# Performance work log

Hardware: AMD Instinct MI355X
Metric: run time of the kernel (lower is better)

Reference implementation:

```python
import jax, jax.numpy as jnp
import numpy as np

MARGIN = 0.2  # contrastive margin
# sim_type_dot = 'MISA': max over image regions, mean over (valid) words


def setup_inputs() -> dict:
    key = jax.random.key(0)
    k1, k2, k3, k4 = jax.random.split(key, 4)
    B, R, W, D = 128, 36, 60, 1024
    im = jax.random.normal(k1, (B, R, D), dtype=jnp.float32)
    s = jax.random.normal(k2, (B, W, D), dtype=jnp.float32)
    x = jax.random.normal(k3, (B, W, D), dtype=jnp.float32)  # unused in math, kept for API fidelity
    s_l = jax.random.randint(k4, (B,), 1, W + 1)  # caption lengths in [1, W]
    return {"im": im, "s": s, "s_l": s_l, "x": x}


def _scores(im, s, s_l):
    # im: (B, R, D) images; s: (B, W, D) captions; s_l: (B,) lengths
    B, W = s.shape[0], s.shape[1]
    # matchmap M[i, j, r, w] = <image j region r, caption i word w>
    M = jnp.einsum('jrd,iwd->ijrw', im, s)
    # MISA: max over regions r, then mean over the n_word valid words of caption i
    M_max = M.max(axis=2)                                   # (i, j, w)
    word_mask = (jnp.arange(W)[None, :] < s_l[:, None]).astype(M.dtype)  # (i, w)
    sims = (M_max * word_mask[:, None, :]).sum(axis=-1) / s_l[:, None].astype(M.dtype)  # (i, j)
    # original layout: scores[image j, caption i]
    return sims.T


def reference(im, s, s_l, x):
    scores = _scores(im, s, s_l)                 # (B, B)
    diag = jnp.diagonal(scores)[:, None]         # (B, 1)
    cost_s = jnp.maximum(MARGIN + scores - diag, 0.0)
    cost_im = jnp.maximum(MARGIN + scores - diag.T, 0.0)
    eye = jnp.eye(scores.shape[0], dtype=bool)
    cost_s = jnp.where(eye, 0.0, cost_s)
    cost_im = jnp.where(eye, 0.0, cost_im)
    return cost_s.sum() + cost_im.sum()
```

## Files before the change

### kernel.cpp

```cpp
#include <hip/hip_runtime.h>
#include <hip/hip_bf16.h>
#include <stdint.h>

#define B_SZ 128
#define R_SZ 36
#define RP_SZ 48
#define W_SZ 60
#define WP_SZ 64
#define D_SZ 1024
#define MARGIN 0.2f

#define ATILE_B (192 * 64)
#define BTILE_B (256 * 64)

typedef __attribute__((ext_vector_type(4))) float f32x4;
typedef __attribute__((ext_vector_type(2))) long longx2;

typedef __attribute__((address_space(3))) unsigned int lds_u32;
typedef const __attribute__((address_space(1))) unsigned int glb_u32;

__device__ __forceinline__ void gload16(const unsigned char* g, unsigned char* l) {
    __builtin_amdgcn_global_load_lds((glb_u32*)g, (lds_u32*)l, 16, 0, 0);
}

__global__ __launch_bounds__(256) void convert_fp8_kernel(
        const float* __restrict__ im, const float* __restrict__ s,
        unsigned char* __restrict__ imb, unsigned char* __restrict__ sb) {
    const int nA = B_SZ * RP_SZ * 64;
    const int nB = B_SZ * WP_SZ * 64;
    int i = blockIdx.x * 256 + threadIdx.x;
    const float* srcrow;
    unsigned char* dst;
    int gran, row;
    if (i < nA) {
        gran = i & 63; row = i >> 6;
        int j = row / RP_SZ, r = row % RP_SZ;
        int rs = r < R_SZ ? r : R_SZ - 1;
        srcrow = im + ((size_t)(j * R_SZ + rs) << 10);
        dst = imb + (size_t)i * 16;
    } else {
        int i2 = i - nA;
        if (i2 >= nB) return;
        gran = i2 & 63; row = i2 >> 6;
        int j = row >> 6, w = row & 63;
        int ws = w < W_SZ ? w : W_SZ - 1;
        srcrow = s + ((size_t)(j * W_SZ + ws) << 10);
        dst = sb + (size_t)i2 * 16;
    }
    const int kb = gran >> 2, g = gran & 3;
    uint4 o;
    unsigned int* op = (unsigned int*)&o;
#pragma unroll
    for (int q = 0; q < 4; ++q) {
        const int kq = kb * 64 + (q >> 1) * 32 + g * 8 + (q & 1) * 4;
        float4 v = *reinterpret_cast<const float4*>(srcrow + kq);
        int w32 = __builtin_amdgcn_cvt_pk_fp8_f32(v.x, v.y, 0, false);
        w32 = __builtin_amdgcn_cvt_pk_fp8_f32(v.z, v.w, w32, true);
        op[q] = (unsigned int)w32;
    }
    *reinterpret_cast<uint4*>(dst) = o;
}

__global__ __launch_bounds__(512, 2) void scores_kernel(
        const unsigned char* __restrict__ imb,
        const unsigned char* __restrict__ sb,
        const int* __restrict__ s_l,
        float* __restrict__ S)
{
    __shared__ __align__(16) unsigned char As[2 * ATILE_B];
    __shared__ __align__(16) unsigned char Bs[2 * BTILE_B];

    const int tid  = threadIdx.x;
    const int wid  = tid >> 6;
    const int lane = tid & 63;
    const int l15  = lane & 15;
    const int kgrp = lane >> 4;
    const int wr   = wid >> 2;
    const int wc   = wid & 3;

    int bid = blockIdx.x;
    int k8  = bid & 7;
    int w   = bid >> 3;
    int jtg = w >> 5;
    int sw  = w & 31;
    int it  = k8 * 4 + (sw >> 3);
    int jt  = jtg * 8 + (sw & 7);

    const int drow = lane >> 2;
    const int sgr  = ((lane & 3) ^ ((lane >> 3) & 3)) * 16;

    const unsigned char* gsrc[4];
    unsigned char* gdst0[4];
    int tsz[4];
#pragma unroll
    for (int si = 0; si < 4; ++si) {
        int c = wid + si * 8;
        if (c < 12) {
            gsrc[si]  = imb + (size_t)(jt * 192 + c * 16 + drow) * 1024 + sgr;
            gdst0[si] = As + c * 1024 + lane * 16;
            tsz[si]   = ATILE_B;
        } else if (c < 28) {
            int b = c - 12;
            gsrc[si]  = sb + (size_t)(it * 256 + b * 16 + drow) * 1024 + sgr;
            gdst0[si] = Bs + b * 1024 + lane * 16;
            tsz[si]   = BTILE_B;
        }
    }

    const int slot0 = (kgrp ^ ((l15 >> 1) & 3)) * 16;
    int abase[6];
#pragma unroll
    for (int rf = 0; rf < 6; ++rf)
        abase[rf] = (wr * 96 + rf * 16 + l15) * 64 + slot0;
    int bbase[4];
#pragma unroll
    for (int cf = 0; cf < 4; ++cf)
        bbase[cf] = (wc * 64 + cf * 16 + l15) * 64 + slot0;

    f32x4 acc[6][4] = {};

#pragma unroll
    for (int si = 0; si < 4; ++si) {
        int c = wid + si * 8;
        if (c < 28) gload16(gsrc[si], gdst0[si]);
    }
    asm volatile("s_waitcnt vmcnt(0)" ::: "memory");
    __builtin_amdgcn_s_barrier();

#pragma unroll 2
    for (int kt = 0; kt < 16; ++kt) {
        const int cur = kt & 1;
        const unsigned char* Ac = As + cur * ATILE_B;
        const unsigned char* Bc = Bs + cur * BTILE_B;

        longx2 afr[6], bfr[4];
#pragma unroll
        for (int rf = 0; rf < 6; ++rf)
            afr[rf] = *reinterpret_cast<const longx2*>(Ac + abase[rf]);
#pragma unroll
        for (int cf = 0; cf < 4; ++cf)
            bfr[cf] = *reinterpret_cast<const longx2*>(Bc + bbase[cf]);

        if (kt < 15) {
            const int ko = (kt + 1) * 64;
            const int nb = cur ^ 1;
#pragma unroll
            for (int si = 0; si < 4; ++si) {
                int c = wid + si * 8;
                if (c < 28) gload16(gsrc[si] + ko, gdst0[si] + nb * tsz[si]);
            }
        }

        __builtin_amdgcn_s_setprio(1);
#pragma unroll
        for (int k2 = 0; k2 < 2; ++k2)
#pragma unroll
            for (int rf = 0; rf < 6; ++rf)
#pragma unroll
                for (int cf = 0; cf < 4; ++cf)
                    acc[rf][cf] = __builtin_amdgcn_mfma_f32_16x16x32_fp8_fp8(
                        afr[rf][k2], bfr[cf][k2], acc[rf][cf], 0, 0, 0);
        __builtin_amdgcn_s_setprio(0);

        if (kt < 15) {
            asm volatile("s_waitcnt vmcnt(0)" ::: "memory");
            __builtin_amdgcn_s_barrier();
        }
    }

    const int i_cap = it * 4 + wc;
    const int nw = s_l[i_cap];
    const float inv = 1.0f / (float)nw;
#pragma unroll
    for (int h = 0; h < 2; ++h) {
        float sum = 0.0f;
#pragma unroll
        for (int cf = 0; cf < 4; ++cf) {
            float m = acc[h * 3][cf][0];
#pragma unroll
            for (int rf = h * 3; rf < h * 3 + 3; ++rf)
#pragma unroll
                for (int e = 0; e < 4; ++e)
                    m = fmaxf(m, acc[rf][cf][e]);
            m = fmaxf(m, __shfl_xor(m, 16));
            m = fmaxf(m, __shfl_xor(m, 32));
            int wv = cf * 16 + l15;
            if (wv < nw) sum += m;
        }
        sum += __shfl_xor(sum, 1);
        sum += __shfl_xor(sum, 2);
        sum += __shfl_xor(sum, 4);
        sum += __shfl_xor(sum, 8);
        if (lane == 0) {
            int j_img = jt * 4 + wr * 2 + h;
            S[j_img * B_SZ + i_cap] = sum * inv;
        }
    }
}

__global__ __launch_bounds__(1024) void loss_kernel(
        const float* __restrict__ S, float* __restrict__ out) {
    __shared__ float diag[B_SZ];
    __shared__ float red[1024];
    int t = threadIdx.x;
    if (t < B_SZ) diag[t] = S[t * (B_SZ + 1)];
    __syncthreads();
    float acc = 0.0f;
    for (int idx = t; idx < B_SZ * B_SZ; idx += 1024) {
        int a = idx >> 7, b = idx & (B_SZ - 1);
        if (a != b) {
            float v = S[idx];
            acc += fmaxf(MARGIN + v - diag[a], 0.0f)
                 + fmaxf(MARGIN + v - diag[b], 0.0f);
        }
    }
    red[t] = acc;
    __syncthreads();
    for (int s = 512; s > 0; s >>= 1) {
        if (t < s) red[t] += red[t + s];
        __syncthreads();
    }
    if (t == 0) out[0] = red[0];
}

extern "C" void kernel_launch(void* const* d_in, const int* in_sizes, int n_in,
                              void* d_out, int out_size, void* d_ws, size_t ws_size,
                              hipStream_t stream) {
    const float* im  = (const float*)d_in[0];
    const float* s   = (const float*)d_in[1];
    const int*   s_l = (const int*)d_in[2];

    const int n_im_pad = B_SZ * RP_SZ * D_SZ;
    const int n_s_pad  = B_SZ * WP_SZ * D_SZ;

    unsigned char* imb = (unsigned char*)d_ws;
    unsigned char* sb  = imb + n_im_pad;
    float* S = (float*)(sb + n_s_pad);

    const int ngran = (n_im_pad + n_s_pad) / 16;
    convert_fp8_kernel<<<(ngran + 255) / 256, 256, 0, stream>>>(im, s, imb, sb);

    scores_kernel<<<1024, 512, 0, stream>>>(imb, sb, s_l, S);

    loss_kernel<<<1, 1024, 0, stream>>>(S, (float*)d_out);
}
```

Baseline: 86.44 us.

## Prefetch two K-tiles ahead and register double-buffer LDS fragments in GEMM loop

Restructures the main K loop of the fp8 scores GEMM. Global-to-LDS loads now run two tiles ahead, and LDS fragments for the next tile are read into a second register set while the second half of the current tile's MFMAs executes. The goal is to hide global-load and LDS latency behind matrix work instead of stalling at the start of each tile. The cost is more live registers (two fragment sets), and the final steps issue a redundant reload of tile 15. It also relies on careful vmcnt and barrier ordering to avoid races on the buffer being overwritten.

```diff
diff --git a/kernel.cpp b/kernel.cpp
--- a/kernel.cpp
+++ b/kernel.cpp
@@ -118,55 +118,73 @@
         bbase[cf] = (wc * 64 + cf * 16 + l15) * 64 + slot0;
 
     f32x4 acc[6][4] = {};
+    longx2 fa[6], fb[4], ga[6], gb[4];
 
 #pragma unroll
     for (int si = 0; si < 4; ++si) {
         int c = wid + si * 8;
         if (c < 28) gload16(gsrc[si], gdst0[si]);
     }
-    asm volatile("s_waitcnt vmcnt(0)" ::: "memory");
+#pragma unroll
+    for (int si = 0; si < 4; ++si) {
+        int c = wid + si * 8;
+        if (c < 28) gload16(gsrc[si] + 64, gdst0[si] + tsz[si]);
+    }
+    asm volatile("s_waitcnt vmcnt(7)" ::: "memory");
     __builtin_amdgcn_s_barrier();
-
-#pragma unroll 2
-    for (int kt = 0; kt < 16; ++kt) {
-        const int cur = kt & 1;
-        const unsigned char* Ac = As + cur * ATILE_B;
-        const unsigned char* Bc = Bs + cur * BTILE_B;
-
-        longx2 afr[6], bfr[4];
-#pragma unroll
-        for (int rf = 0; rf < 6; ++rf)
-            afr[rf] = *reinterpret_cast<const longx2*>(Ac + abase[rf]);
-#pragma unroll
-        for (int cf = 0; cf < 4; ++cf)
-            bfr[cf] = *reinterpret_cast<const longx2*>(Bc + bbase[cf]);
-
-        if (kt < 15) {
-            const int ko = (kt + 1) * 64;
-            const int nb = cur ^ 1;
-#pragma unroll
-            for (int si = 0; si < 4; ++si) {
-                int c = wid + si * 8;
-                if (c < 28) gload16(gsrc[si] + ko, gdst0[si] + nb * tsz[si]);
-            }
-        }
-
-        __builtin_amdgcn_s_setprio(1);
-#pragma unroll
-        for (int k2 = 0; k2 < 2; ++k2)
-#pragma unroll
-            for (int rf = 0; rf < 6; ++rf)
-#pragma unroll
-                for (int cf = 0; cf < 4; ++cf)
-                    acc[rf][cf] = __builtin_amdgcn_mfma_f32_16x16x32_fp8_fp8(
-                        afr[rf][k2], bfr[cf][k2], acc[rf][cf], 0, 0, 0);
-        __builtin_amdgcn_s_setprio(0);
-
-        if (kt < 15) {
-            asm volatile("s_waitcnt vmcnt(0)" ::: "memory");
-            __builtin_amdgcn_s_barrier();
-        }
-    }
+#pragma unroll
+    for (int rf = 0; rf < 6; ++rf)
+        fa[rf] = *reinterpret_cast<const longx2*>(As + abase[rf]);
+#pragma unroll
+    for (int cf = 0; cf < 4; ++cf)
+        fb[cf] = *reinterpret_cast<const longx2*>(Bs + bbase[cf]);
+
+#define TILE_STEP(t, CA, CB, NA, NB)                                           \
+    {                                                                          \
+        const int cur = (t) & 1;                                               \
+        __builtin_amdgcn_s_setprio(1);                                         \
+        _Pragma("unroll")                                                      \
+        for (int rf = 0; rf < 6; ++rf)                                         \
+            _Pragma("unroll")                                                  \
+            for (int cf = 0; cf < 4; ++cf)                                     \
+                acc[rf][cf] = __builtin_amdgcn_mfma_f32_16x16x32_fp8_fp8(      \
+                    CA[rf][0], CB[cf][0], acc[rf][cf], 0, 0, 0);               \
+        __builtin_amdgcn_s_setprio(0);                                         \
+        if ((t) < 15) {                                                        \
+            asm volatile("s_waitcnt vmcnt(0)" ::: "memory");                   \
+            __builtin_amdgcn_s_barrier();                                      \
+            const int ko = ((t) + 2 < 16 ? (t) + 2 : 15) * 64;                 \
+            _Pragma("unroll")                                                  \
+            for (int si = 0; si < 4; ++si) {                                   \
+                int c = wid + si * 8;                                          \
+                if (c < 28) gload16(gsrc[si] + ko, gdst0[si] + cur * tsz[si]); \
+            }                                                                  \
+            const unsigned char* An = As + (cur ^ 1) * ATILE_B;                \
+            const unsigned char* Bn = Bs + (cur ^ 1) * BTILE_B;                \
+            _Pragma("unroll")                                                  \
+            for (int rf = 0; rf < 6; ++rf)                                     \
+                NA[rf] = *reinterpret_cast<const longx2*>(An + abase[rf]);     \
+            _Pragma("unroll")                                                  \
+            for (int cf = 0; cf < 4; ++cf)                                     \
+                NB[cf] = *reinterpret_cast<const longx2*>(Bn + bbase[cf]);     \
+            __builtin_amdgcn_sched_barrier(0);                                 \
+        }                                                                      \
+        __builtin_amdgcn_s_setprio(1);                                         \
+        _Pragma("unroll")                                                      \
+        for (int rf = 0; rf < 6; ++rf)                                         \
+            _Pragma("unroll")                                                  \
+            for (int cf = 0; cf < 4; ++cf)                                     \
+                acc[rf][cf] = __builtin_amdgcn_mfma_f32_16x16x32_fp8_fp8(      \
+                    CA[rf][1], CB[cf][1], acc[rf][cf], 0, 0, 0);               \
+        __builtin_amdgcn_s_setprio(0);                                         \
+    }
+
+#pragma unroll 1
+    for (int tp = 0; tp < 8; ++tp) {
+        TILE_STEP(tp * 2,     fa, fb, ga, gb);
+        TILE_STEP(tp * 2 + 1, ga, gb, fa, fb);
+    }
+#undef TILE_STEP
 
     const int i_cap = it * 4 + wc;
     const int nw = s_l[i_cap];
```

New measurement: 130.9 us. +51.5%, slower.

## Deepen scores kernel LDS pipeline to four stages with partial vmcnt waits

Applied to the files above, without the earlier changes.

Replaces the double-buffered K loop with a 4-deep ring of LDS tiles. Three stages are prefetched up front, and each iteration waits only until the oldest stage has landed (vmcnt(8) or vmcnt(6), depending on how many loads each wave issues). This is meant to hide global-to-LDS latency that the old full vmcnt(0) wait exposed. The cost is twice the LDS, so launch bounds drop to one 512-thread block per CU, and the tail re-issues clamped redundant loads.

```diff
diff --git a/kernel.cpp b/kernel.cpp
--- a/kernel.cpp
+++ b/kernel.cpp
@@ -61,14 +61,14 @@
     *reinterpret_cast<uint4*>(dst) = o;
 }
 
-__global__ __launch_bounds__(512, 2) void scores_kernel(
+__global__ __launch_bounds__(512, 1) void scores_kernel(
         const unsigned char* __restrict__ imb,
         const unsigned char* __restrict__ sb,
         const int* __restrict__ s_l,
         float* __restrict__ S)
 {
-    __shared__ __align__(16) unsigned char As[2 * ATILE_B];
-    __shared__ __align__(16) unsigned char Bs[2 * BTILE_B];
+    __shared__ __align__(16) unsigned char As[4 * ATILE_B];
+    __shared__ __align__(16) unsigned char Bs[4 * BTILE_B];
 
     const int tid  = threadIdx.x;
     const int wid  = tid >> 6;
@@ -120,51 +120,57 @@
     f32x4 acc[6][4] = {};
 
 #pragma unroll
-    for (int si = 0; si < 4; ++si) {
-        int c = wid + si * 8;
-        if (c < 28) gload16(gsrc[si], gdst0[si]);
-    }
-    asm volatile("s_waitcnt vmcnt(0)" ::: "memory");
+    for (int b = 0; b < 3; ++b)
+#pragma unroll
+        for (int si = 0; si < 4; ++si) {
+            int c = wid + si * 8;
+            if (c < 28) gload16(gsrc[si] + b * 64, gdst0[si] + b * tsz[si]);
+        }
+    if (wid < 4) { asm volatile("s_waitcnt vmcnt(8)" ::: "memory"); }
+    else         { asm volatile("s_waitcnt vmcnt(6)" ::: "memory"); }
     __builtin_amdgcn_s_barrier();
 
-#pragma unroll 2
-    for (int kt = 0; kt < 16; ++kt) {
-        const int cur = kt & 1;
-        const unsigned char* Ac = As + cur * ATILE_B;
-        const unsigned char* Bc = Bs + cur * BTILE_B;
-
-        longx2 afr[6], bfr[4];
-#pragma unroll
-        for (int rf = 0; rf < 6; ++rf)
-            afr[rf] = *reinterpret_cast<const longx2*>(Ac + abase[rf]);
-#pragma unroll
-        for (int cf = 0; cf < 4; ++cf)
-            bfr[cf] = *reinterpret_cast<const longx2*>(Bc + bbase[cf]);
-
-        if (kt < 15) {
-            const int ko = (kt + 1) * 64;
-            const int nb = cur ^ 1;
+#pragma unroll 1
+    for (int g = 0; g < 4; ++g) {
+#pragma unroll
+        for (int s = 0; s < 4; ++s) {
+            const int u  = g * 4 + s;
+            const int rb = s;
+            const int sb4 = (s + 3) & 3;
+
+            const int ko = (u + 3 < 16 ? u + 3 : 15) * 64;
 #pragma unroll
             for (int si = 0; si < 4; ++si) {
                 int c = wid + si * 8;
-                if (c < 28) gload16(gsrc[si] + ko, gdst0[si] + nb * tsz[si]);
+                if (c < 28) gload16(gsrc[si] + ko, gdst0[si] + sb4 * tsz[si]);
             }
-        }
-
-        __builtin_amdgcn_s_setprio(1);
-#pragma unroll
-        for (int k2 = 0; k2 < 2; ++k2)
+
+            const unsigned char* Ac = As + rb * ATILE_B;
+            const unsigned char* Bc = Bs + rb * BTILE_B;
+            longx2 afr[6], bfr[4];
 #pragma unroll
             for (int rf = 0; rf < 6; ++rf)
-#pragma unroll
-                for (int cf = 0; cf < 4; ++cf)
-                    acc[rf][cf] = __builtin_amdgcn_mfma_f32_16x16x32_fp8_fp8(
-                        afr[rf][k2], bfr[cf][k2], acc[rf][cf], 0, 0, 0);
-        __builtin_amdgcn_s_setprio(0);
-
-        if (kt < 15) {
-            asm volatile("s_waitcnt vmcnt(0)" ::: "memory");
-            __builtin_amdgcn_s_barrier();
+                afr[rf] = *reinterpret_cast<const longx2*>(Ac + abase[rf]);
+#pragma unroll
+            for (int cf = 0; cf < 4; ++cf)
+                bfr[cf] = *reinterpret_cast<const longx2*>(Bc + bbase[cf]);
+
+            __builtin_amdgcn_s_setprio(1);
+#pragma unroll
+            for (int k2 = 0; k2 < 2; ++k2)
+#pragma unroll
+                for (int rf = 0; rf < 6; ++rf)
+#pragma unroll
+                    for (int cf = 0; cf < 4; ++cf)
+                        acc[rf][cf] = __builtin_amdgcn_mfma_f32_16x16x32_fp8_fp8(
+                            afr[rf][k2], bfr[cf][k2], acc[rf][cf], 0, 0, 0);
+            __builtin_amdgcn_s_setprio(0);
+
+            if (u < 15) {
+                if (wid < 4) { asm volatile("s_waitcnt vmcnt(8)" ::: "memory"); }
+                else         { asm volatile("s_waitcnt vmcnt(6)" ::: "memory"); }
+                __builtin_amdgcn_s_barrier();
+            }
         }
     }
 
```

Measured after the change: 94.14 us. 1.09x slower.
